# Optimization experiments

Measured on AMD Instinct MI355X. Metric: run time of the kernel, lower is better.

## Reference

```python
import jax, jax.numpy as jnp
import numpy as np
from jax import lax

B, N, F = 64, 768, 256
P, T, K = 64, 16, 3  # per_lead, after_lead, kernel_size


def setup_inputs() -> dict:
    key = jax.random.key(0)
    k1, k2, k3, k4, k5 = jax.random.split(key, 5)
    x = jax.random.normal(k1, (B, N, F), dtype=jnp.float32)
    adj = jax.random.uniform(k2, (B, N, N), dtype=jnp.float32)
    fan_in = P * 1 * K
    bound = 1.0 / np.sqrt(fan_in)
    conv_w = jax.random.uniform(k3, (T, P, 1, K), minval=-bound, maxval=bound, dtype=jnp.float32)
    conv_b = jax.random.uniform(k4, (T,), minval=-bound, maxval=bound, dtype=jnp.float32)
    re_param = jax.random.normal(k5, (K, 1), dtype=jnp.float32)
    return {"x": x, "adj": adj, "conv_w": conv_w, "conv_b": conv_b, "re_param": re_param}


def reference(x, adj, conv_w, conv_b, re_param):
    b, n, f = x.shape
    t, p, _, k = conv_w.shape
    L = n // p  # number of leads
    # feature pooling: [B, P, L, F] -conv(1,k)-> [B, T, L, F]
    x4 = x.reshape(b, p, L, f)
    pad = (k - 1) // 2
    y = lax.conv_general_dilated(
        x4, conv_w, window_strides=(1, 1), padding=[(0, 0), (pad, pad)],
        dimension_numbers=("NCHW", "OIHW", "NCHW"))
    y = y + conv_b[None, :, None, None]
    pooled_x = y.reshape(b, t * L, f)
    # assignment matrix s = conv_w @ re_param  -> [T, P]
    s = jnp.einsum("tpik,kj->tp", conv_w, re_param)
    # block-diagonal coarsening: for every (lead_i, lead_j) block do s @ A_ij @ s^T
    adj5 = adj.reshape(b, L, p, L, p)
    pooled = jnp.einsum("tp,blpmq,uq->bltmu", s, adj5, s)
    pooled_adj = pooled.reshape(b, L * t, L * t)
    return pooled_x, pooled_adj
```

## Files before the change

### kernel.cpp

```cpp
#include <hip/hip_runtime.h>

#define B_ 64
#define N_ 768
#define F_ 256
#define P_ 64
#define T_ 16
#define K_ 3
#define L_ 12
#define TSTRIDE 772

__global__ __launch_bounds__(256) void fused_pool_kernel(
    const float* __restrict__ x, const float* __restrict__ adj,
    const float* __restrict__ conv_w, const float* __restrict__ conv_b,
    const float* __restrict__ re_param,
    float* __restrict__ out_x, float* __restrict__ out_adj)
{
    __shared__ float sT[P_][T_];
    __shared__ float tmp[T_][TSTRIDE];

    const int blk  = blockIdx.x;
    const int role = blk & 1;
    const int idx  = blk >> 1;
    const int b = idx / L_, l = idx % L_;
    const int tid = threadIdx.x;

    if (role == 1) {
        const int f = tid;
        const float* xb = x + (size_t)b * N_ * F_ + (size_t)l * F_;

        float acc[T_];
        #pragma unroll
        for (int t = 0; t < T_; ++t) acc[t] = conv_b[t];

        for (int p = 0; p < P_; ++p) {
            const float* row = xb + (size_t)p * (L_ * F_);
            const float xm = (f > 0)      ? row[f - 1] : 0.f;
            const float x0 = row[f];
            const float xp = (f < F_ - 1) ? row[f + 1] : 0.f;
            const float* wp = conv_w + p * K_;
            #pragma unroll
            for (int t = 0; t < T_; ++t) {
                const float w0 = wp[t * (P_ * K_) + 0];
                const float w1 = wp[t * (P_ * K_) + 1];
                const float w2 = wp[t * (P_ * K_) + 2];
                acc[t] = fmaf(xm, w0, fmaf(x0, w1, fmaf(xp, w2, acc[t])));
            }
        }
        float* ob = out_x + (size_t)b * (T_ * L_) * F_ + f;
        #pragma unroll
        for (int t = 0; t < T_; ++t)
            ob[(size_t)(t * L_ + l) * F_] = acc[t];
        return;
    }

    const float r0 = re_param[0], r1 = re_param[1], r2 = re_param[2];
    for (int i = tid; i < P_ * T_; i += 256) {
        const int p = i >> 4, t = i & 15;
        const float* wv = conv_w + (size_t)t * (P_ * K_) + (size_t)p * K_;
        sT[p][t] = wv[0] * r0 + wv[1] * r1 + wv[2] * r2;
    }
    __syncthreads();

    const int w  = tid >> 6;
    const int ct = tid & 63;

    float acc[4][12];
    #pragma unroll
    for (int j = 0; j < 4; ++j)
        #pragma unroll
        for (int c = 0; c < 12; ++c) acc[j][c] = 0.f;

    const float* ab = adj + (size_t)b * N_ * N_ + (size_t)(l * P_) * N_;
    for (int p = 0; p < P_; ++p) {
        const float* row = ab + (size_t)p * N_;
        const float4 a0 = *(const float4*)&row[ct * 4];
        const float4 a1 = *(const float4*)&row[ct * 4 + 256];
        const float4 a2 = *(const float4*)&row[ct * 4 + 512];
        #pragma unroll
        for (int j = 0; j < 4; ++j) {
            const float sv = sT[p][4 * w + j];
            acc[j][0]  = fmaf(sv, a0.x, acc[j][0]);
            acc[j][1]  = fmaf(sv, a0.y, acc[j][1]);
            acc[j][2]  = fmaf(sv, a0.z, acc[j][2]);
            acc[j][3]  = fmaf(sv, a0.w, acc[j][3]);
            acc[j][4]  = fmaf(sv, a1.x, acc[j][4]);
            acc[j][5]  = fmaf(sv, a1.y, acc[j][5]);
            acc[j][6]  = fmaf(sv, a1.z, acc[j][6]);
            acc[j][7]  = fmaf(sv, a1.w, acc[j][7]);
            acc[j][8]  = fmaf(sv, a2.x, acc[j][8]);
            acc[j][9]  = fmaf(sv, a2.y, acc[j][9]);
            acc[j][10] = fmaf(sv, a2.z, acc[j][10]);
            acc[j][11] = fmaf(sv, a2.w, acc[j][11]);
        }
    }
    #pragma unroll
    for (int j = 0; j < 4; ++j) {
        #pragma unroll
        for (int i = 0; i < 3; ++i) {
            float4 v;
            v.x = acc[j][i * 4 + 0]; v.y = acc[j][i * 4 + 1];
            v.z = acc[j][i * 4 + 2]; v.w = acc[j][i * 4 + 3];
            *(float4*)&tmp[4 * w + j][ct * 4 + i * 256] = v;
        }
    }
    __syncthreads();

    const int t = tid >> 4, u = tid & 15;
    float sum[L_];
    #pragma unroll
    for (int m = 0; m < L_; ++m) sum[m] = 0.f;

    for (int q4 = 0; q4 < P_; q4 += 4) {
        const float s0 = sT[q4 + 0][u];
        const float s1 = sT[q4 + 1][u];
        const float s2 = sT[q4 + 2][u];
        const float s3 = sT[q4 + 3][u];
        #pragma unroll
        for (int m = 0; m < L_; ++m) {
            const float4 tv = *(const float4*)&tmp[t][m * P_ + q4];
            sum[m] = fmaf(tv.x, s0, fmaf(tv.y, s1, fmaf(tv.z, s2, fmaf(tv.w, s3, sum[m]))));
        }
    }

    float* ob = out_adj + (size_t)b * (L_ * T_) * (L_ * T_)
                        + (size_t)(l * T_ + t) * (L_ * T_) + u;
    #pragma unroll
    for (int m = 0; m < L_; ++m)
        ob[m * T_] = sum[m];
}

extern "C" void kernel_launch(void* const* d_in, const int* in_sizes, int n_in,
                              void* d_out, int out_size, void* d_ws, size_t ws_size,
                              hipStream_t stream) {
    (void)in_sizes; (void)n_in; (void)out_size; (void)d_ws; (void)ws_size;
    const float* x        = (const float*)d_in[0];
    const float* adj      = (const float*)d_in[1];
    const float* conv_w   = (const float*)d_in[2];
    const float* conv_b   = (const float*)d_in[3];
    const float* re_param = (const float*)d_in[4];

    float* pooled_x   = (float*)d_out;
    float* pooled_adj = (float*)d_out + (size_t)B_ * (T_ * L_) * F_;

    fused_pool_kernel<<<B_ * L_ * 2, 256, 0, stream>>>(
        x, adj, conv_w, conv_b, re_param, pooled_x, pooled_adj);
}
```

Measured before the change: 76.12 us.

## Split adjacency coarsening into column chunks and drop block-wide barrier

```diff
diff --git a/kernel.cpp b/kernel.cpp
--- a/kernel.cpp
+++ b/kernel.cpp
@@ -7,7 +7,9 @@
 #define T_ 16
 #define K_ 3
 #define L_ 12
-#define TSTRIDE 772
+#define CH_ 3
+#define CCOLS 256
+#define TSTR 260
 
 __global__ __launch_bounds__(256) void fused_pool_kernel(
     const float* __restrict__ x, const float* __restrict__ adj,
@@ -16,15 +18,14 @@
     float* __restrict__ out_x, float* __restrict__ out_adj)
 {
     __shared__ float sT[P_][T_];
-    __shared__ float tmp[T_][TSTRIDE];
+    __shared__ float tmp[T_][TSTR];
 
-    const int blk  = blockIdx.x;
-    const int role = blk & 1;
-    const int idx  = blk >> 1;
-    const int b = idx / L_, l = idx % L_;
+    const int blk = blockIdx.x;
     const int tid = threadIdx.x;
 
-    if (role == 1) {
+    if ((blk & 3) == 3) {
+        const int idx = blk >> 2;
+        const int b = idx / L_, l = idx % L_;
         const int f = tid;
         const float* xb = x + (size_t)b * N_ * F_ + (size_t)l * F_;
 
@@ -53,9 +54,15 @@
         return;
     }
 
+    const int aidx = (blk >> 2) * CH_ + (blk & 3);
+    const int b = aidx / (L_ * CH_);
+    const int rem = aidx % (L_ * CH_);
+    const int l = rem / CH_;
+    const int i = rem % CH_;
+
     const float r0 = re_param[0], r1 = re_param[1], r2 = re_param[2];
-    for (int i = tid; i < P_ * T_; i += 256) {
-        const int p = i >> 4, t = i & 15;
+    for (int j = tid; j < P_ * T_; j += 256) {
+        const int p = j >> 4, t = j & 15;
         const float* wv = conv_w + (size_t)t * (P_ * K_) + (size_t)p * K_;
         sT[p][t] = wv[0] * r0 + wv[1] * r1 + wv[2] * r2;
     }
@@ -64,51 +71,47 @@
     const int w  = tid >> 6;
     const int ct = tid & 63;
 
-    float acc[4][12];
+    float acc[4][4];
     #pragma unroll
     for (int j = 0; j < 4; ++j)
         #pragma unroll
-        for (int c = 0; c < 12; ++c) acc[j][c] = 0.f;
+        for (int r = 0; r < 4; ++r) acc[j][r] = 0.f;
 
-    const float* ab = adj + (size_t)b * N_ * N_ + (size_t)(l * P_) * N_;
+    const float* ab = adj + (size_t)b * N_ * N_ + (size_t)(l * P_) * N_
+                          + (size_t)i * CCOLS + 4 * ct;
+    #pragma unroll 4
     for (int p = 0; p < P_; ++p) {
-        const float* row = ab + (size_t)p * N_;
-        const float4 a0 = *(const float4*)&row[ct * 4];
-        const float4 a1 = *(const float4*)&row[ct * 4 + 256];
-        const float4 a2 = *(const float4*)&row[ct * 4 + 512];
-        #pragma unroll
-        for (int j = 0; j < 4; ++j) {
-            const float sv = sT[p][4 * w + j];
-            acc[j][0]  = fmaf(sv, a0.x, acc[j][0]);
-            acc[j][1]  = fmaf(sv, a0.y, acc[j][1]);
-            acc[j][2]  = fmaf(sv, a0.z, acc[j][2]);
-            acc[j][3]  = fmaf(sv, a0.w, acc[j][3]);
-            acc[j][4]  = fmaf(sv, a1.x, acc[j][4]);
-            acc[j][5]  = fmaf(sv, a1.y, acc[j][5]);
-            acc[j][6]  = fmaf(sv, a1.z, acc[j][6]);
-            acc[j][7]  = fmaf(sv, a1.w, acc[j][7]);
-            acc[j][8]  = fmaf(sv, a2.x, acc[j][8]);
-            acc[j][9]  = fmaf(sv, a2.y, acc[j][9]);
-            acc[j][10] = fmaf(sv, a2.z, acc[j][10]);
-            acc[j][11] = fmaf(sv, a2.w, acc[j][11]);
-        }
+        const float4 a  = *(const float4*)(ab + (size_t)p * N_);
+        const float4 sv = *(const float4*)&sT[p][4 * w];
+        acc[0][0] = fmaf(sv.x, a.x, acc[0][0]);
+        acc[0][1] = fmaf(sv.x, a.y, acc[0][1]);
+        acc[0][2] = fmaf(sv.x, a.z, acc[0][2]);
+        acc[0][3] = fmaf(sv.x, a.w, acc[0][3]);
+        acc[1][0] = fmaf(sv.y, a.x, acc[1][0]);
+        acc[1][1] = fmaf(sv.y, a.y, acc[1][1]);
+        acc[1][2] = fmaf(sv.y, a.z, acc[1][2]);
+        acc[1][3] = fmaf(sv.y, a.w, acc[1][3]);
+        acc[2][0] = fmaf(sv.z, a.x, acc[2][0]);
+        acc[2][1] = fmaf(sv.z, a.y, acc[2][1]);
+        acc[2][2] = fmaf(sv.z, a.z, acc[2][2]);
+        acc[2][3] = fmaf(sv.z, a.w, acc[2][3]);
+        acc[3][0] = fmaf(sv.w, a.x, acc[3][0]);
+        acc[3][1] = fmaf(sv.w, a.y, acc[3][1]);
+        acc[3][2] = fmaf(sv.w, a.z, acc[3][2]);
+        acc[3][3] = fmaf(sv.w, a.w, acc[3][3]);
     }
+
     #pragma unroll
     for (int j = 0; j < 4; ++j) {
-        #pragma unroll
-        for (int i = 0; i < 3; ++i) {
-            float4 v;
-            v.x = acc[j][i * 4 + 0]; v.y = acc[j][i * 4 + 1];
-            v.z = acc[j][i * 4 + 2]; v.w = acc[j][i * 4 + 3];
-            *(float4*)&tmp[4 * w + j][ct * 4 + i * 256] = v;
-        }
+        float4 v;
+        v.x = acc[j][0]; v.y = acc[j][1]; v.z = acc[j][2]; v.w = acc[j][3];
+        *(float4*)&tmp[4 * w + j][4 * ct] = v;
     }
-    __syncthreads();
+    asm volatile("s_waitcnt lgkmcnt(0)" ::: "memory");
+    __builtin_amdgcn_sched_barrier(0);
 
     const int t = tid >> 4, u = tid & 15;
-    float sum[L_];
-    #pragma unroll
-    for (int m = 0; m < L_; ++m) sum[m] = 0.f;
+    float sum[4] = {0.f, 0.f, 0.f, 0.f};
 
     for (int q4 = 0; q4 < P_; q4 += 4) {
         const float s0 = sT[q4 + 0][u];
@@ -116,17 +119,18 @@
         const float s2 = sT[q4 + 2][u];
         const float s3 = sT[q4 + 3][u];
         #pragma unroll
-        for (int m = 0; m < L_; ++m) {
-            const float4 tv = *(const float4*)&tmp[t][m * P_ + q4];
-            sum[m] = fmaf(tv.x, s0, fmaf(tv.y, s1, fmaf(tv.z, s2, fmaf(tv.w, s3, sum[m]))));
+        for (int mi = 0; mi < 4; ++mi) {
+            const float4 tv = *(const float4*)&tmp[t][mi * P_ + q4];
+            sum[mi] = fmaf(tv.x, s0, fmaf(tv.y, s1, fmaf(tv.z, s2, fmaf(tv.w, s3, sum[mi]))));
         }
     }
 
     float* ob = out_adj + (size_t)b * (L_ * T_) * (L_ * T_)
-                        + (size_t)(l * T_ + t) * (L_ * T_) + u;
+                        + (size_t)(l * T_ + t) * (L_ * T_)
+                        + (size_t)(4 * i) * T_ + u;
     #pragma unroll
-    for (int m = 0; m < L_; ++m)
-        ob[m * T_] = sum[m];
+    for (int mi = 0; mi < 4; ++mi)
+        ob[mi * T_] = sum[mi];
 }
 
 extern "C" void kernel_launch(void* const* d_in, const int* in_sizes, int n_in,
@@ -142,6 +146,6 @@
     float* pooled_x   = (float*)d_out;
     float* pooled_adj = (float*)d_out + (size_t)B_ * (T_ * L_) * F_;
 
-    fused_pool_kernel<<<B_ * L_ * 2, 256, 0, stream>>>(
+    fused_pool_kernel<<<B_ * L_ * 4, 256, 0, stream>>>(
         x, adj, conv_w, conv_b, re_param, pooled_x, pooled_adj);
 }
```

Result: slower. 108.1 us (+42.1%).

## Remap block schedule and restructure adj first-stage to load each element once

Applied to the files above, without the earlier changes.

```diff
diff --git a/kernel.cpp b/kernel.cpp
--- a/kernel.cpp
+++ b/kernel.cpp
@@ -7,7 +7,7 @@
 #define T_ 16
 #define K_ 3
 #define L_ 12
-#define TSTRIDE 772
+#define TSTR 772
 
 __global__ __launch_bounds__(256) void fused_pool_kernel(
     const float* __restrict__ x, const float* __restrict__ adj,
@@ -16,15 +16,16 @@
     float* __restrict__ out_x, float* __restrict__ out_adj)
 {
     __shared__ float sT[P_][T_];
-    __shared__ float tmp[T_][TSTRIDE];
+    __shared__ float tmp[T_][TSTR];
 
-    const int blk  = blockIdx.x;
-    const int role = blk & 1;
-    const int idx  = blk >> 1;
-    const int b = idx / L_, l = idx % L_;
+    const int g  = blockIdx.x;
+    const int Lg = (g & 7) * 192 + (g >> 3);
+    const int b  = Lg / 24;
+    const int r  = Lg % 24;
     const int tid = threadIdx.x;
 
-    if (role == 1) {
+    if (r >= L_) {
+        const int l = r - L_;
         const int f = tid;
         const float* xb = x + (size_t)b * N_ * F_ + (size_t)l * F_;
 
@@ -32,18 +33,25 @@
         #pragma unroll
         for (int t = 0; t < T_; ++t) acc[t] = conv_b[t];
 
-        for (int p = 0; p < P_; ++p) {
-            const float* row = xb + (size_t)p * (L_ * F_);
-            const float xm = (f > 0)      ? row[f - 1] : 0.f;
-            const float x0 = row[f];
-            const float xp = (f < F_ - 1) ? row[f + 1] : 0.f;
-            const float* wp = conv_w + p * K_;
+        for (int p0 = 0; p0 < P_; p0 += 2) {
+            float xm[2], x0[2], xp[2];
             #pragma unroll
-            for (int t = 0; t < T_; ++t) {
-                const float w0 = wp[t * (P_ * K_) + 0];
-                const float w1 = wp[t * (P_ * K_) + 1];
-                const float w2 = wp[t * (P_ * K_) + 2];
-                acc[t] = fmaf(xm, w0, fmaf(x0, w1, fmaf(xp, w2, acc[t])));
+            for (int rr = 0; rr < 2; ++rr) {
+                const float* row = xb + (size_t)(p0 + rr) * (L_ * F_);
+                xm[rr] = (f > 0)      ? row[f - 1] : 0.f;
+                x0[rr] = row[f];
+                xp[rr] = (f < F_ - 1) ? row[f + 1] : 0.f;
+            }
+            #pragma unroll
+            for (int rr = 0; rr < 2; ++rr) {
+                const float* wp = conv_w + (p0 + rr) * K_;
+                #pragma unroll
+                for (int t = 0; t < T_; ++t) {
+                    const float w0 = wp[t * (P_ * K_) + 0];
+                    const float w1 = wp[t * (P_ * K_) + 1];
+                    const float w2 = wp[t * (P_ * K_) + 2];
+                    acc[t] = fmaf(xm[rr], w0, fmaf(x0[rr], w1, fmaf(xp[rr], w2, acc[t])));
+                }
             }
         }
         float* ob = out_x + (size_t)b * (T_ * L_) * F_ + f;
@@ -53,55 +61,57 @@
         return;
     }
 
+    const int l = r;
+
     const float r0 = re_param[0], r1 = re_param[1], r2 = re_param[2];
-    for (int i = tid; i < P_ * T_; i += 256) {
-        const int p = i >> 4, t = i & 15;
+    for (int j = tid; j < P_ * T_; j += 256) {
+        const int p = j >> 4, t = j & 15;
         const float* wv = conv_w + (size_t)t * (P_ * K_) + (size_t)p * K_;
         sT[p][t] = wv[0] * r0 + wv[1] * r1 + wv[2] * r2;
     }
     __syncthreads();
 
-    const int w  = tid >> 6;
-    const int ct = tid & 63;
+    float acc[T_][3];
+    #pragma unroll
+    for (int t = 0; t < T_; ++t)
+        #pragma unroll
+        for (int c = 0; c < 3; ++c) acc[t][c] = 0.f;
 
-    float acc[4][12];
-    #pragma unroll
-    for (int j = 0; j < 4; ++j)
+    const float* ab = adj + (size_t)b * N_ * N_ + (size_t)(l * P_) * N_ + tid;
+    for (int p0 = 0; p0 < P_; p0 += 8) {
+        float a[8][3];
         #pragma unroll
-        for (int c = 0; c < 12; ++c) acc[j][c] = 0.f;
-
-    const float* ab = adj + (size_t)b * N_ * N_ + (size_t)(l * P_) * N_;
-    for (int p = 0; p < P_; ++p) {
-        const float* row = ab + (size_t)p * N_;
-        const float4 a0 = *(const float4*)&row[ct * 4];
-        const float4 a1 = *(const float4*)&row[ct * 4 + 256];
-        const float4 a2 = *(const float4*)&row[ct * 4 + 512];
+        for (int rr = 0; rr < 8; ++rr) {
+            const float* row = ab + (size_t)(p0 + rr) * N_;
+            a[rr][0] = row[0];
+            a[rr][1] = row[256];
+            a[rr][2] = row[512];
+        }
         #pragma unroll
-        for (int j = 0; j < 4; ++j) {
-            const float sv = sT[p][4 * w + j];
-            acc[j][0]  = fmaf(sv, a0.x, acc[j][0]);
-            acc[j][1]  = fmaf(sv, a0.y, acc[j][1]);
-            acc[j][2]  = fmaf(sv, a0.z, acc[j][2]);
-            acc[j][3]  = fmaf(sv, a0.w, acc[j][3]);
-            acc[j][4]  = fmaf(sv, a1.x, acc[j][4]);
-            acc[j][5]  = fmaf(sv, a1.y, acc[j][5]);
-            acc[j][6]  = fmaf(sv, a1.z, acc[j][6]);
-            acc[j][7]  = fmaf(sv, a1.w, acc[j][7]);
-            acc[j][8]  = fmaf(sv, a2.x, acc[j][8]);
-            acc[j][9]  = fmaf(sv, a2.y, acc[j][9]);
-            acc[j][10] = fmaf(sv, a2.z, acc[j][10]);
-            acc[j][11] = fmaf(sv, a2.w, acc[j][11]);
+        for (int rr = 0; rr < 8; ++rr) {
+            #pragma unroll
+            for (int j = 0; j < 4; ++j) {
+                const float4 sv = *(const float4*)&sT[p0 + rr][4 * j];
+                acc[4*j+0][0] = fmaf(sv.x, a[rr][0], acc[4*j+0][0]);
+                acc[4*j+0][1] = fmaf(sv.x, a[rr][1], acc[4*j+0][1]);
+                acc[4*j+0][2] = fmaf(sv.x, a[rr][2], acc[4*j+0][2]);
+                acc[4*j+1][0] = fmaf(sv.y, a[rr][0], acc[4*j+1][0]);
+                acc[4*j+1][1] = fmaf(sv.y, a[rr][1], acc[4*j+1][1]);
+                acc[4*j+1][2] = fmaf(sv.y, a[rr][2], acc[4*j+1][2]);
+                acc[4*j+2][0] = fmaf(sv.z, a[rr][0], acc[4*j+2][0]);
+                acc[4*j+2][1] = fmaf(sv.z, a[rr][1], acc[4*j+2][1]);
+                acc[4*j+2][2] = fmaf(sv.z, a[rr][2], acc[4*j+2][2]);
+                acc[4*j+3][0] = fmaf(sv.w, a[rr][0], acc[4*j+3][0]);
+                acc[4*j+3][1] = fmaf(sv.w, a[rr][1], acc[4*j+3][1]);
+                acc[4*j+3][2] = fmaf(sv.w, a[rr][2], acc[4*j+3][2]);
+            }
         }
     }
     #pragma unroll
-    for (int j = 0; j < 4; ++j) {
-        #pragma unroll
-        for (int i = 0; i < 3; ++i) {
-            float4 v;
-            v.x = acc[j][i * 4 + 0]; v.y = acc[j][i * 4 + 1];
-            v.z = acc[j][i * 4 + 2]; v.w = acc[j][i * 4 + 3];
-            *(float4*)&tmp[4 * w + j][ct * 4 + i * 256] = v;
-        }
+    for (int t = 0; t < T_; ++t) {
+        tmp[t][tid]       = acc[t][0];
+        tmp[t][tid + 256] = acc[t][1];
+        tmp[t][tid + 512] = acc[t][2];
     }
     __syncthreads();
 
```

New measurement: 87.14 us. +14.5%, slower.

## Split fused pooling into multi-kernel pipeline with global intermediate buffer

Applied to the files above, without the earlier changes.

```diff
diff --git a/kernel.cpp b/kernel.cpp
--- a/kernel.cpp
+++ b/kernel.cpp
@@ -7,9 +7,135 @@
 #define T_ 16
 #define K_ 3
 #define L_ 12
+#define C4_ 192
+#define PA_BLOCKS 576
+#define CONV_BLOCKS 768
+#define WS_NEED_BYTES (8192 + (size_t)B_ * L_ * T_ * N_ * 4)
+
+__global__ void compute_s_kernel(const float* __restrict__ conv_w,
+                                 const float* __restrict__ re_param,
+                                 float* __restrict__ ws) {
+    const int j = blockIdx.x * 256 + threadIdx.x;
+    if (j < P_ * T_) {
+        const int p = j >> 4, t = j & 15;
+        const float* w = conv_w + (size_t)t * (P_ * K_) + (size_t)p * K_;
+        const float s = w[0] * re_param[0] + w[1] * re_param[1] + w[2] * re_param[2];
+        ws[p * T_ + t] = s;
+        ws[1024 + t * P_ + p] = s;
+    }
+}
+
+__global__ __launch_bounds__(256) void streamA_kernel(
+    const float* __restrict__ x, const float* __restrict__ adj,
+    const float* __restrict__ conv_w, const float* __restrict__ conv_b,
+    const float* __restrict__ sT, float* __restrict__ tmp,
+    float* __restrict__ out_x)
+{
+    const int blk = blockIdx.x;
+    const int tid = threadIdx.x;
+
+    if (blk < PA_BLOCKS) {
+        const int j  = blk * 256 + tid;
+        const int c4 = j % C4_;
+        const int bl = j / C4_;
+        const float* arow = adj + (size_t)bl * (P_ * N_) + 4 * c4;
+
+        float acc[T_][4];
+        #pragma unroll
+        for (int t = 0; t < T_; ++t) {
+            acc[t][0] = 0.f; acc[t][1] = 0.f; acc[t][2] = 0.f; acc[t][3] = 0.f;
+        }
+
+        for (int p0 = 0; p0 < P_; p0 += 4) {
+            float4 a[4];
+            #pragma unroll
+            for (int r = 0; r < 4; ++r)
+                a[r] = *(const float4*)(arow + (size_t)(p0 + r) * N_);
+            #pragma unroll
+            for (int r = 0; r < 4; ++r) {
+                const float* sp = sT + (p0 + r) * T_;
+                #pragma unroll
+                for (int t = 0; t < T_; ++t) {
+                    const float sv = sp[t];
+                    acc[t][0] = fmaf(sv, a[r].x, acc[t][0]);
+                    acc[t][1] = fmaf(sv, a[r].y, acc[t][1]);
+                    acc[t][2] = fmaf(sv, a[r].z, acc[t][2]);
+                    acc[t][3] = fmaf(sv, a[r].w, acc[t][3]);
+                }
+            }
+        }
+        float* trow = tmp + (size_t)bl * (T_ * N_) + 4 * c4;
+        #pragma unroll
+        for (int t = 0; t < T_; ++t) {
+            float4 v;
+            v.x = acc[t][0]; v.y = acc[t][1]; v.z = acc[t][2]; v.w = acc[t][3];
+            *(float4*)(trow + (size_t)t * N_) = v;
+        }
+        return;
+    }
+
+    const int idx = blk - PA_BLOCKS;
+    const int b = idx / L_, l = idx % L_;
+    const int f = tid;
+    const float* xb = x + (size_t)b * N_ * F_ + (size_t)l * F_;
+
+    float acc[T_];
+    #pragma unroll
+    for (int t = 0; t < T_; ++t) acc[t] = conv_b[t];
+
+    for (int p0 = 0; p0 < P_; p0 += 2) {
+        float xm[2], x0[2], xp[2];
+        #pragma unroll
+        for (int rr = 0; rr < 2; ++rr) {
+            const float* row = xb + (size_t)(p0 + rr) * (L_ * F_);
+            xm[rr] = (f > 0)      ? row[f - 1] : 0.f;
+            x0[rr] = row[f];
+            xp[rr] = (f < F_ - 1) ? row[f + 1] : 0.f;
+        }
+        #pragma unroll
+        for (int rr = 0; rr < 2; ++rr) {
+            const float* wp = conv_w + (p0 + rr) * K_;
+            #pragma unroll
+            for (int t = 0; t < T_; ++t) {
+                const float w0 = wp[t * (P_ * K_) + 0];
+                const float w1 = wp[t * (P_ * K_) + 1];
+                const float w2 = wp[t * (P_ * K_) + 2];
+                acc[t] = fmaf(xm[rr], w0, fmaf(x0[rr], w1, fmaf(xp[rr], w2, acc[t])));
+            }
+        }
+    }
+    float* ob = out_x + (size_t)b * (T_ * L_) * F_ + f;
+    #pragma unroll
+    for (int t = 0; t < T_; ++t)
+        ob[(size_t)(t * L_ + l) * F_] = acc[t];
+}
+
+__global__ __launch_bounds__(256) void streamB_kernel(
+    const float* __restrict__ tmp, const float* __restrict__ sU,
+    float* __restrict__ out_adj)
+{
+    const int blk = blockIdx.x;
+    const int m  = blk % L_;
+    const int bl = blk / L_;
+    const int t = threadIdx.x >> 4, u = threadIdx.x & 15;
+
+    const float* trow = tmp + (size_t)bl * (T_ * N_) + (size_t)t * N_ + m * P_;
+    const float* srow = sU + u * P_;
+
+    float sum = 0.f;
+    #pragma unroll
+    for (int q4 = 0; q4 < P_; q4 += 4) {
+        const float4 tv = *(const float4*)(trow + q4);
+        const float4 sv = *(const float4*)(srow + q4);
+        sum = fmaf(tv.x, sv.x, fmaf(tv.y, sv.y, fmaf(tv.z, sv.z, fmaf(tv.w, sv.w, sum))));
+    }
+
+    out_adj[((size_t)(bl / L_) * (L_ * T_) + (bl % L_) * T_ + t) * (L_ * T_)
+            + m * T_ + u] = sum;
+}
+
 #define TSTRIDE 772
-
-__global__ __launch_bounds__(256) void fused_pool_kernel(
+__global__ __launch_bounds__(256) void fallback_fused_kernel(
     const float* __restrict__ x, const float* __restrict__ adj,
     const float* __restrict__ conv_w, const float* __restrict__ conv_b,
     const float* __restrict__ re_param,
@@ -27,11 +153,9 @@
     if (role == 1) {
         const int f = tid;
         const float* xb = x + (size_t)b * N_ * F_ + (size_t)l * F_;
-
         float acc[T_];
         #pragma unroll
         for (int t = 0; t < T_; ++t) acc[t] = conv_b[t];
-
         for (int p = 0; p < P_; ++p) {
             const float* row = xb + (size_t)p * (L_ * F_);
             const float xm = (f > 0)      ? row[f - 1] : 0.f;
@@ -40,10 +164,9 @@
             const float* wp = conv_w + p * K_;
             #pragma unroll
             for (int t = 0; t < T_; ++t) {
-                const float w0 = wp[t * (P_ * K_) + 0];
-                const float w1 = wp[t * (P_ * K_) + 1];
-                const float w2 = wp[t * (P_ * K_) + 2];
-                acc[t] = fmaf(xm, w0, fmaf(x0, w1, fmaf(xp, w2, acc[t])));
+                acc[t] = fmaf(xm, wp[t * (P_ * K_)],
+                         fmaf(x0, wp[t * (P_ * K_) + 1],
+                         fmaf(xp, wp[t * (P_ * K_) + 2], acc[t])));
             }
         }
         float* ob = out_x + (size_t)b * (T_ * L_) * F_ + f;
@@ -63,12 +186,11 @@
 
     const int w  = tid >> 6;
     const int ct = tid & 63;
-
     float acc[4][12];
     #pragma unroll
-    for (int j = 0; j < 4; ++j)
-        #pragma unroll
-        for (int c = 0; c < 12; ++c) acc[j][c] = 0.f;
+    for (int jj = 0; jj < 4; ++jj)
+        #pragma unroll
+        for (int c = 0; c < 12; ++c) acc[jj][c] = 0.f;
 
     const float* ab = adj + (size_t)b * N_ * N_ + (size_t)(l * P_) * N_;
     for (int p = 0; p < P_; ++p) {
@@ -77,62 +199,59 @@
         const float4 a1 = *(const float4*)&row[ct * 4 + 256];
         const float4 a2 = *(const float4*)&row[ct * 4 + 512];
         #pragma unroll
-        for (int j = 0; j < 4; ++j) {
-            const float sv = sT[p][4 * w + j];
-            acc[j][0]  = fmaf(sv, a0.x, acc[j][0]);
-            acc[j][1]  = fmaf(sv, a0.y, acc[j][1]);
-            acc[j][2]  = fmaf(sv, a0.z, acc[j][2]);
-            acc[j][3]  = fmaf(sv, a0.w, acc[j][3]);
-            acc[j][4]  = fmaf(sv, a1.x, acc[j][4]);
-            acc[j][5]  = fmaf(sv, a1.y, acc[j][5]);
-            acc[j][6]  = fmaf(sv, a1.z, acc[j][6]);
-            acc[j][7]  = fmaf(sv, a1.w, acc[j][7]);
-            acc[j][8]  = fmaf(sv, a2.x, acc[j][8]);
-            acc[j][9]  = fmaf(sv, a2.y, acc[j][9]);
-            acc[j][10] = fmaf(sv, a2.z, acc[j][10]);
-            acc[j][11] = fmaf(sv, a2.w, acc[j][11]);
-        }
-    }
-    #pragma unroll
-    for (int j = 0; j < 4; ++j) {
+        for (int jj = 0; jj < 4; ++jj) {
+            const float sv = sT[p][4 * w + jj];
+            acc[jj][0]  = fmaf(sv, a0.x, acc[jj][0]);
+            acc[jj][1]  = fmaf(sv, a0.y, acc[jj][1]);
+            acc[jj][2]  = fmaf(sv, a0.z, acc[jj][2]);
+            acc[jj][3]  = fmaf(sv, a0.w, acc[jj][3]);
+            acc[jj][4]  = fmaf(sv, a1.x, acc[jj][4]);
+            acc[jj][5]  = fmaf(sv, a1.y, acc[jj][5]);
+            acc[jj][6]  = fmaf(sv, a1.z, acc[jj][6]);
+            acc[jj][7]  = fmaf(sv, a1.w, acc[jj][7]);
+            acc[jj][8]  = fmaf(sv, a2.x, acc[jj][8]);
+            acc[jj][9]  = fmaf(sv, a2.y, acc[jj][9]);
+            acc[jj][10] = fmaf(sv, a2.z, acc[jj][10]);
+            acc[jj][11] = fmaf(sv, a2.w, acc[jj][11]);
+        }
+    }
+    #pragma unroll
+    for (int jj = 0; jj < 4; ++jj)
         #pragma unroll
         for (int i = 0; i < 3; ++i) {
             float4 v;
-            v.x = acc[j][i * 4 + 0]; v.y = acc[j][i * 4 + 1];
-            v.z = acc[j][i * 4 + 2]; v.w = acc[j][i * 4 + 3];
-            *(float4*)&tmp[4 * w + j][ct * 4 + i * 256] = v;
-        }
-    }
+            v.x = acc[jj][i * 4 + 0]; v.y = acc[jj][i * 4 + 1];
+            v.z = acc[jj][i * 4 + 2]; v.w = acc[jj][i * 4 + 3];
+            *(float4*)&tmp[4 * w + jj][ct * 4 + i * 256] = v;
+        }
     __syncthreads();
 
     const int t = tid >> 4, u = tid & 15;
     float sum[L_];
     #pragma unroll
-    for (int m = 0; m < L_; ++m) sum[m] = 0.f;
-
+    for (int mm = 0; mm < L_; ++mm) sum[mm] = 0.f;
     for (int q4 = 0; q4 < P_; q4 += 4) {
         const float s0 = sT[q4 + 0][u];
         const float s1 = sT[q4 + 1][u];
         const float s2 = sT[q4 + 2][u];
         const float s3 = sT[q4 + 3][u];
         #pragma unroll
-        for (int m = 0; m < L_; ++m) {
-            const float4 tv = *(const float4*)&tmp[t][m * P_ + q4];
-            sum[m] = fmaf(tv.x, s0, fmaf(tv.y, s1, fmaf(tv.z, s2, fmaf(tv.w, s3, sum[m]))));
-        }
-    }
-
+        for (int mm = 0; mm < L_; ++mm) {
+            const float4 tv = *(const float4*)&tmp[t][mm * P_ + q4];
+            sum[mm] = fmaf(tv.x, s0, fmaf(tv.y, s1, fmaf(tv.z, s2, fmaf(tv.w, s3, sum[mm]))));
+        }
+    }
     float* ob = out_adj + (size_t)b * (L_ * T_) * (L_ * T_)
                         + (size_t)(l * T_ + t) * (L_ * T_) + u;
     #pragma unroll
-    for (int m = 0; m < L_; ++m)
-        ob[m * T_] = sum[m];
+    for (int mm = 0; mm < L_; ++mm)
+        ob[mm * T_] = sum[mm];
 }
 
 extern "C" void kernel_launch(void* const* d_in, const int* in_sizes, int n_in,
                               void* d_out, int out_size, void* d_ws, size_t ws_size,
                               hipStream_t stream) {
-    (void)in_sizes; (void)n_in; (void)out_size; (void)d_ws; (void)ws_size;
+    (void)in_sizes; (void)n_in; (void)out_size;
     const float* x        = (const float*)d_in[0];
     const float* adj      = (const float*)d_in[1];
     const float* conv_w   = (const float*)d_in[2];
@@ -142,6 +261,17 @@
     float* pooled_x   = (float*)d_out;
     float* pooled_adj = (float*)d_out + (size_t)B_ * (T_ * L_) * F_;
 
-    fused_pool_kernel<<<B_ * L_ * 2, 256, 0, stream>>>(
-        x, adj, conv_w, conv_b, re_param, pooled_x, pooled_adj);
-}
+    if (ws_size >= WS_NEED_BYTES) {
+        float* ws  = (float*)d_ws;
+        float* sT  = ws;
+        float* sU  = ws + 1024;
+        float* tmp = ws + 2048;
+        compute_s_kernel<<<4, 256, 0, stream>>>(conv_w, re_param, ws);
+        streamA_kernel<<<PA_BLOCKS + CONV_BLOCKS, 256, 0, stream>>>(
+            x, adj, conv_w, conv_b, sT, tmp, pooled_x);
+        streamB_kernel<<<B_ * L_ * L_, 256, 0, stream>>>(tmp, sU, pooled_adj);
+    } else {
+        fallback_fused_kernel<<<B_ * L_ * 2, 256, 0, stream>>>(
+            x, adj, conv_w, conv_b, re_param, pooled_x, pooled_adj);
+    }
+}
```

Measured after the change: 146.1 us. +91.9%, slower.
